# Performance work log

Hardware: AMD Instinct MI355X
Metric: run time of the kernel (lower is better)

## Reference

```python
import jax, jax.numpy as jnp
import numpy as np

C = 64

def setup_inputs() -> dict:
    key = jax.random.key(0)
    ks = jax.random.split(key, 4)
    B, H, W = 16, 256, 256
    feature = jax.random.normal(ks[0], (B, C, H, W), dtype=jnp.float32)
    confidence = jax.random.uniform(ks[1], (B, 1, H, W), dtype=jnp.float32)
    # input_proj: Conv1d(C, C, k=1) -> weight squeezed to [C, C]; state_proj likewise
    Wi = jax.random.normal(ks[2], (C, C), dtype=jnp.float32) * 0.05
    bi = jnp.zeros((C,), dtype=jnp.float32)
    Ws = jax.random.normal(ks[3], (C, C), dtype=jnp.float32) * 0.05
    bs = jnp.zeros((C,), dtype=jnp.float32)
    bias = jnp.zeros((C,), dtype=jnp.float32)
    return {"feature": feature, "confidence": confidence, "Wi": Wi, "bi": bi,
            "Ws": Ws, "bs": bs, "bias": bias}


def reference(feature, confidence, Wi, bi, Ws, bs, bias):
    # direction = 'lr' (propagate left-to-right along width)
    B, Cc, H, W = feature.shape
    # [B,C,H,W] -> [B*H, C, W]  (independent rows)
    seq = feature.transpose(0, 2, 1, 3).reshape(B * H, Cc, W)
    gate = confidence.transpose(0, 2, 1, 3).reshape(B * H, 1, W)
    # pointwise input projection (Conv1d k=1)
    proj = jnp.einsum('oc,ncw->now', Wi, seq) + bi[None, :, None]
    xs = (jnp.moveaxis(proj, -1, 0), jnp.moveaxis(gate, -1, 0))  # [W,N,C], [W,N,1]

    def step(prev, x):
        p_t, g_t = x                      # [N,C], [N,1]
        rec = (prev * g_t) @ Ws.T + bs    # state_proj on gated previous state
        cur = jax.nn.relu(p_t + rec + bias)
        return cur, cur

    init = jnp.zeros((B * H, Cc), dtype=feature.dtype)
    _, ys = jax.lax.scan(step, init, xs)  # [W, N, C]
    out = jnp.moveaxis(ys, 0, -1).reshape(B, H, Cc, W).transpose(0, 2, 1, 3)
    return out
```

## Files before the change

### kernel.cpp

```cpp
#include <hip/hip_runtime.h>
#include <hip/hip_bf16.h>


typedef __attribute__((ext_vector_type(8))) short short8;
typedef __attribute__((ext_vector_type(4))) short short4v;
typedef __attribute__((ext_vector_type(2))) short short2v;
typedef __attribute__((ext_vector_type(4))) float f32x4;

union FragU { unsigned int u[4]; short8 v; };
union PkU { unsigned int u; short2v s2; };

__device__ __forceinline__ unsigned int pk2(float a, float b) {
    unsigned short lo = __bfloat16_as_ushort(__float2bfloat16(a));
    unsigned short hi = __bfloat16_as_ushort(__float2bfloat16(b));
    return (unsigned int)lo | ((unsigned int)hi << 16);
}
__device__ __forceinline__ float b2f(short x) {
    return __uint_as_float(((unsigned int)(unsigned short)x) << 16);
}

__device__ __forceinline__ int fsi(int w, int n, int c) {
    return (w * 1024 + n * 64 + c) ^ ((n & 7) << 3);
}
__device__ __forceinline__ int ogi(int o, int n, int w) {
    return (o * 256 + n * 16 + w) ^ ((((o >> 2) ^ (n >> 2)) & 3) << 2);
}

#define BAR() asm volatile("s_waitcnt lgkmcnt(0)\n\ts_barrier" ::: "memory")

template<int V> struct Ic { static constexpr int value = V; };

__global__ __launch_bounds__(256, 1) void dp_v5_kernel(
    const float* __restrict__ feat, const float* __restrict__ conf,
    const float* __restrict__ Wi, const float* __restrict__ bi,
    const float* __restrict__ Ws, const float* __restrict__ bs,
    const float* __restrict__ bias, float* __restrict__ outp)
{
    __shared__ unsigned short fs[2][16384];
    __shared__ unsigned short og[2][16384];

    const int tid = threadIdx.x;
    const int lane = tid & 63;
    const int wid = tid >> 6;
    const int l15 = lane & 15, g4 = lane >> 4;
    const int nb = blockIdx.x;
    const int b = nb >> 4, h0 = (nb & 15) * 16;

    const float* fb = feat + (size_t)b * 64 * 65536 + (size_t)h0 * 256;

    if (wid == 0) {
        const float* gb = conf + ((size_t)(b * 256) + h0 + l15) * 256;

        FragU Ai[4][2], As[4][2];
        #pragma unroll
        for (int t = 0; t < 4; ++t)
            #pragma unroll
            for (int h = 0; h < 2; ++h) {
                const float* si = Wi + (16 * t + l15) * 64 + 32 * h + g4 * 8;
                const float* ss = Ws + (16 * t + l15) * 64;
                #pragma unroll
                for (int d = 0; d < 4; ++d) {
                    Ai[t][h].u[d] = pk2(si[2 * d], si[2 * d + 1]);
                    const int c0 = 16 * (2 * h + (d >> 1)) + 4 * g4 + 2 * (d & 1);
                    As[t][h].u[d] = pk2(ss[c0], ss[c0 + 1]);
                }
            }
        f32x4 binit[4];
        #pragma unroll
        for (int t = 0; t < 4; ++t)
            #pragma unroll
            for (int r = 0; r < 4; ++r) {
                int o = 16 * t + 4 * g4 + r;
                binit[t][r] = bi[o] + bs[o] + bias[o];
            }

        f32x4 gqA[4], gqB[4];
        #pragma unroll
        for (int q = 0; q < 4; ++q) gqA[q] = *(const f32x4*)(gb + 4 * q);

        FragU S0, S1;
        #pragma unroll
        for (int d = 0; d < 4; ++d) { S0.u[d] = 0u; S1.u[d] = 0u; }

        float curE[4][4];

        BAR();

        auto run_chunk = [&](auto pc, int cc) {
            constexpr int P = decltype(pc)::value;
            f32x4 (&gqc)[4] = P ? gqB : gqA;
            f32x4 (&gqn)[4] = P ? gqA : gqB;
            const int w0 = cc * 16;
            #pragma unroll
            for (int u = 0; u < 16; ++u) {
                short8 F0 = *(const short8*)&fs[P][fsi(u, l15, 8 * g4)];
                short8 F1 = *(const short8*)&fs[P][fsi(u, l15, 32 + 8 * g4)];

                if (u == 2 && cc < 15) {
                    #pragma unroll
                    for (int q = 0; q < 4; ++q)
                        gqn[q] = *(const f32x4*)(gb + w0 + 16 + 4 * q);
                }

                f32x4 a0 = binit[0], a1 = binit[1], a2 = binit[2], a3 = binit[3];
                a0 = __builtin_amdgcn_mfma_f32_16x16x32_bf16(Ai[0][0].v, F0, a0, 0, 0, 0);
                a1 = __builtin_amdgcn_mfma_f32_16x16x32_bf16(Ai[1][0].v, F0, a1, 0, 0, 0);
                a2 = __builtin_amdgcn_mfma_f32_16x16x32_bf16(Ai[2][0].v, F0, a2, 0, 0, 0);
                a3 = __builtin_amdgcn_mfma_f32_16x16x32_bf16(Ai[3][0].v, F0, a3, 0, 0, 0);
                a0 = __builtin_amdgcn_mfma_f32_16x16x32_bf16(Ai[0][1].v, F1, a0, 0, 0, 0);
                a1 = __builtin_amdgcn_mfma_f32_16x16x32_bf16(Ai[1][1].v, F1, a1, 0, 0, 0);
                a2 = __builtin_amdgcn_mfma_f32_16x16x32_bf16(Ai[2][1].v, F1, a2, 0, 0, 0);
                a3 = __builtin_amdgcn_mfma_f32_16x16x32_bf16(Ai[3][1].v, F1, a3, 0, 0, 0);
                a0 = __builtin_amdgcn_mfma_f32_16x16x32_bf16(As[0][0].v, S0.v, a0, 0, 0, 0);
                a1 = __builtin_amdgcn_mfma_f32_16x16x32_bf16(As[1][0].v, S0.v, a1, 0, 0, 0);
                a2 = __builtin_amdgcn_mfma_f32_16x16x32_bf16(As[2][0].v, S0.v, a2, 0, 0, 0);
                a3 = __builtin_amdgcn_mfma_f32_16x16x32_bf16(As[3][0].v, S0.v, a3, 0, 0, 0);
                a0 = __builtin_amdgcn_mfma_f32_16x16x32_bf16(As[0][1].v, S1.v, a0, 0, 0, 0);
                a1 = __builtin_amdgcn_mfma_f32_16x16x32_bf16(As[1][1].v, S1.v, a1, 0, 0, 0);
                a2 = __builtin_amdgcn_mfma_f32_16x16x32_bf16(As[2][1].v, S1.v, a2, 0, 0, 0);
                a3 = __builtin_amdgcn_mfma_f32_16x16x32_bf16(As[3][1].v, S1.v, a3, 0, 0, 0);

                float cur[4][4];
                #pragma unroll
                for (int r = 0; r < 4; ++r) {
                    cur[0][r] = fmaxf(a0[r], 0.f);
                    cur[1][r] = fmaxf(a1[r], 0.f);
                    cur[2][r] = fmaxf(a2[r], 0.f);
                    cur[3][r] = fmaxf(a3[r], 0.f);
                }

                if ((u & 1) == 0) {
                    #pragma unroll
                    for (int t = 0; t < 4; ++t)
                        #pragma unroll
                        for (int r = 0; r < 4; ++r) curE[t][r] = cur[t][r];
                } else {
                    #pragma unroll
                    for (int t = 0; t < 4; ++t)
                        #pragma unroll
                        for (int r = 0; r < 4; ++r) {
                            PkU pk; pk.u = pk2(curE[t][r], cur[t][r]);
                            *(short2v*)&og[P][ogi(16 * t + 4 * g4 + r, l15, u - 1)] = pk.s2;
                        }
                }

                if (!(cc == 15 && u == 15)) {
                    float gv = (u < 15) ? gqc[(u + 1) >> 2][(u + 1) & 3] : gqn[0][0];
                    float g0[4], g1[4], g2[4], g3[4];
                    #pragma unroll
                    for (int r = 0; r < 4; ++r) {
                        g0[r] = cur[0][r] * gv; g1[r] = cur[1][r] * gv;
                        g2[r] = cur[2][r] * gv; g3[r] = cur[3][r] * gv;
                    }
                    S0.u[0] = pk2(g0[0], g0[1]); S0.u[1] = pk2(g0[2], g0[3]);
                    S0.u[2] = pk2(g1[0], g1[1]); S0.u[3] = pk2(g1[2], g1[3]);
                    S1.u[0] = pk2(g2[0], g2[1]); S1.u[1] = pk2(g2[2], g2[3]);
                    S1.u[2] = pk2(g3[0], g3[1]); S1.u[3] = pk2(g3[2], g3[3]);
                }
            }
            BAR();
        };

        #pragma unroll 1
        for (int c2 = 0; c2 < 8; ++c2) {
            run_chunk(Ic<0>{}, 2 * c2);
            run_chunk(Ic<1>{}, 2 * c2 + 1);
        }
    } else if (wid <= 2) {
        const int cb2 = (wid - 1) * 16;
        const int n = lane & 15;

        auto stage = [&](int buf, int w0) {
            f32x4 ra[4][2][4];
            #pragma unroll
            for (int pi = 0; pi < 4; ++pi) {
                const int cp = cb2 + 4 * pi + g4;
                const float* p0 = fb + (size_t)(2 * cp) * 65536 + n * 256 + w0;
                #pragma unroll
                for (int row = 0; row < 2; ++row)
                    #pragma unroll
                    for (int q = 0; q < 4; ++q)
                        ra[pi][row][q] = *(const f32x4*)(p0 + row * 65536 + 4 * q);
            }
            #pragma unroll
            for (int pi = 0; pi < 4; ++pi) {
                const int cp = cb2 + 4 * pi + g4;
                #pragma unroll
                for (int q = 0; q < 4; ++q)
                    #pragma unroll
                    for (int e = 0; e < 4; ++e) {
                        PkU pk; pk.u = pk2(ra[pi][0][q][e], ra[pi][1][q][e]);
                        *(short2v*)&fs[buf][fsi(4 * q + e, n, 2 * cp)] = pk.s2;
                    }
            }
        };

        stage(0, 0);
        BAR();
        #pragma unroll 1
        for (int cc = 0; cc < 16; ++cc) {
            if (cc < 15) stage((cc + 1) & 1, (cc + 1) * 16);
            BAR();
        }
    } else {
        const int n = (lane >> 2) & 15, wq = lane & 3;
        float* const ob = outp + ((size_t)(b * 64) * 256 + h0 + n) * 256 + 4 * wq;

        auto drain = [&](int buf, int wpr) {
            #pragma unroll 8
            for (int o = 0; o < 64; ++o) {
                short4v d = *(const short4v*)&og[buf][ogi(o, n, 4 * wq)];
                f32x4 o4 = { b2f(d.x), b2f(d.y), b2f(d.z), b2f(d.w) };
                *(f32x4*)(ob + (size_t)o * 65536 + wpr) = o4;
            }
        };

        BAR();
        #pragma unroll 1
        for (int cc = 0; cc < 16; ++cc) {
            if (cc > 0) drain((cc - 1) & 1, (cc - 1) * 16);
            BAR();
        }
        drain(1, 240);
    }
}

extern "C" void kernel_launch(void* const* d_in, const int* in_sizes, int n_in,
                              void* d_out, int out_size, void* d_ws, size_t ws_size,
                              hipStream_t stream) {
    const float* feat = (const float*)d_in[0];
    const float* conf = (const float*)d_in[1];
    const float* Wi   = (const float*)d_in[2];
    const float* bi   = (const float*)d_in[3];
    const float* Ws   = (const float*)d_in[4];
    const float* bs   = (const float*)d_in[5];
    const float* bias = (const float*)d_in[6];
    float* out = (float*)d_out;
    (void)d_ws; (void)ws_size; (void)in_sizes; (void)n_in; (void)out_size;

    dp_v5_kernel<<<256, 256, 0, stream>>>(feat, conf, Wi, bi, Ws, bs, bias, out);
}
```

Measured before the change: 184.3 us.

## Move input projection GEMM to producer waves, feed fp32 projections via LDS

The input projection (Wi·x + biases) leaves the serial recurrence wave and moves to the two loader waves. They compute it with MFMA per half-chunk of 8 columns and store fp32 results in a swizzled LDS buffer. The recurrence wave then only runs the Ws MFMAs per step, shortening the critical dependent chain. In exchange the loaders issue scalar strided global loads, and barriers now occur every half-chunk, so the drain wave splits its work across four barriers per chunk pair.

After: 204.6 us. 11.0% more time.

```diff
diff --git a/kernel.cpp b/kernel.cpp
--- a/kernel.cpp
+++ b/kernel.cpp
@@ -19,8 +19,8 @@
     return __uint_as_float(((unsigned int)(unsigned short)x) << 16);
 }
 
-__device__ __forceinline__ int fsi(int w, int n, int c) {
-    return (w * 1024 + n * 64 + c) ^ ((n & 7) << 3);
+__device__ __forceinline__ int psi(int w, int n, int o) {
+    return (w * 1024 + n * 64 + o) ^ ((n & 7) << 2) ^ ((w & 7) << 2);
 }
 __device__ __forceinline__ int ogi(int o, int n, int w) {
     return (o * 256 + n * 16 + w) ^ ((((o >> 2) ^ (n >> 2)) & 3) << 2);
@@ -30,13 +30,13 @@
 
 template<int V> struct Ic { static constexpr int value = V; };
 
-__global__ __launch_bounds__(256, 1) void dp_v5_kernel(
+__global__ __launch_bounds__(256, 1) void dp_v8_kernel(
     const float* __restrict__ feat, const float* __restrict__ conf,
     const float* __restrict__ Wi, const float* __restrict__ bi,
     const float* __restrict__ Ws, const float* __restrict__ bs,
     const float* __restrict__ bias, float* __restrict__ outp)
 {
-    __shared__ unsigned short fs[2][16384];
+    __shared__ float ps[2][8192];
     __shared__ unsigned short og[2][16384];
 
     const int tid = threadIdx.x;
@@ -51,28 +51,18 @@
     if (wid == 0) {
         const float* gb = conf + ((size_t)(b * 256) + h0 + l15) * 256;
 
-        FragU Ai[4][2], As[4][2];
+        FragU As[4][2];
         #pragma unroll
         for (int t = 0; t < 4; ++t)
             #pragma unroll
             for (int h = 0; h < 2; ++h) {
-                const float* si = Wi + (16 * t + l15) * 64 + 32 * h + g4 * 8;
                 const float* ss = Ws + (16 * t + l15) * 64;
                 #pragma unroll
                 for (int d = 0; d < 4; ++d) {
-                    Ai[t][h].u[d] = pk2(si[2 * d], si[2 * d + 1]);
                     const int c0 = 16 * (2 * h + (d >> 1)) + 4 * g4 + 2 * (d & 1);
                     As[t][h].u[d] = pk2(ss[c0], ss[c0 + 1]);
                 }
             }
-        f32x4 binit[4];
-        #pragma unroll
-        for (int t = 0; t < 4; ++t)
-            #pragma unroll
-            for (int r = 0; r < 4; ++r) {
-                int o = 16 * t + 4 * g4 + r;
-                binit[t][r] = bi[o] + bs[o] + bias[o];
-            }
 
         f32x4 gqA[4], gqB[4];
         #pragma unroll
@@ -86,31 +76,32 @@
 
         BAR();
 
-        auto run_chunk = [&](auto pc, int cc) {
-            constexpr int P = decltype(pc)::value;
-            f32x4 (&gqc)[4] = P ? gqB : gqA;
-            f32x4 (&gqn)[4] = P ? gqA : gqB;
-            const int w0 = cc * 16;
-            #pragma unroll
-            for (int u = 0; u < 16; ++u) {
-                short8 F0 = *(const short8*)&fs[P][fsi(u, l15, 8 * g4)];
-                short8 F1 = *(const short8*)&fs[P][fsi(u, l15, 32 + 8 * g4)];
-
-                if (u == 2 && cc < 15) {
+        auto run_half = [&](auto Hc, auto Qc, int C) {
+            constexpr int H = decltype(Hc)::value;
+            constexpr int Q = decltype(Qc)::value;
+            f32x4 (&gqc)[4] = Q ? gqB : gqA;
+            f32x4 (&gqn)[4] = Q ? gqA : gqB;
+            f32x4 accP[2][4];
+            #pragma unroll
+            for (int t = 0; t < 4; ++t)
+                accP[0][t] = *(const f32x4*)&ps[H][psi(0, l15, 16 * t + 4 * g4)];
+            #pragma unroll
+            for (int u = 0; u < 8; ++u) {
+                const int wl = H * 8 + u;
+                if (u < 7) {
+                    #pragma unroll
+                    for (int t = 0; t < 4; ++t)
+                        accP[(u + 1) & 1][t] =
+                            *(const f32x4*)&ps[H][psi(u + 1, l15, 16 * t + 4 * g4)];
+                }
+                if (H == 0 && u == 4 && C < 15) {
                     #pragma unroll
                     for (int q = 0; q < 4; ++q)
-                        gqn[q] = *(const f32x4*)(gb + w0 + 16 + 4 * q);
-                }
-
-                f32x4 a0 = binit[0], a1 = binit[1], a2 = binit[2], a3 = binit[3];
-                a0 = __builtin_amdgcn_mfma_f32_16x16x32_bf16(Ai[0][0].v, F0, a0, 0, 0, 0);
-                a1 = __builtin_amdgcn_mfma_f32_16x16x32_bf16(Ai[1][0].v, F0, a1, 0, 0, 0);
-                a2 = __builtin_amdgcn_mfma_f32_16x16x32_bf16(Ai[2][0].v, F0, a2, 0, 0, 0);
-                a3 = __builtin_amdgcn_mfma_f32_16x16x32_bf16(Ai[3][0].v, F0, a3, 0, 0, 0);
-                a0 = __builtin_amdgcn_mfma_f32_16x16x32_bf16(Ai[0][1].v, F1, a0, 0, 0, 0);
-                a1 = __builtin_amdgcn_mfma_f32_16x16x32_bf16(Ai[1][1].v, F1, a1, 0, 0, 0);
-                a2 = __builtin_amdgcn_mfma_f32_16x16x32_bf16(Ai[2][1].v, F1, a2, 0, 0, 0);
-                a3 = __builtin_amdgcn_mfma_f32_16x16x32_bf16(Ai[3][1].v, F1, a3, 0, 0, 0);
+                        gqn[q] = *(const f32x4*)(gb + (C + 1) * 16 + 4 * q);
+                }
+
+                f32x4 a0 = accP[u & 1][0], a1 = accP[u & 1][1];
+                f32x4 a2 = accP[u & 1][2], a3 = accP[u & 1][3];
                 a0 = __builtin_amdgcn_mfma_f32_16x16x32_bf16(As[0][0].v, S0.v, a0, 0, 0, 0);
                 a1 = __builtin_amdgcn_mfma_f32_16x16x32_bf16(As[1][0].v, S0.v, a1, 0, 0, 0);
                 a2 = __builtin_amdgcn_mfma_f32_16x16x32_bf16(As[2][0].v, S0.v, a2, 0, 0, 0);
@@ -129,7 +120,7 @@
                     cur[3][r] = fmaxf(a3[r], 0.f);
                 }
 
-                if ((u & 1) == 0) {
+                if ((wl & 1) == 0) {
                     #pragma unroll
                     for (int t = 0; t < 4; ++t)
                         #pragma unroll
@@ -140,12 +131,12 @@
                         #pragma unroll
                         for (int r = 0; r < 4; ++r) {
                             PkU pk; pk.u = pk2(curE[t][r], cur[t][r]);
-                            *(short2v*)&og[P][ogi(16 * t + 4 * g4 + r, l15, u - 1)] = pk.s2;
+                            *(short2v*)&og[Q][ogi(16 * t + 4 * g4 + r, l15, wl - 1)] = pk.s2;
                         }
                 }
 
-                if (!(cc == 15 && u == 15)) {
-                    float gv = (u < 15) ? gqc[(u + 1) >> 2][(u + 1) & 3] : gqn[0][0];
+                if (!(C == 15 && wl == 15)) {
+                    float gv = (wl < 15) ? gqc[(wl + 1) >> 2][(wl + 1) & 3] : gqn[0][0];
                     float g0[4], g1[4], g2[4], g3[4];
                     #pragma unroll
                     for (int r = 0; r < 4; ++r) {
@@ -163,52 +154,88 @@
 
         #pragma unroll 1
         for (int c2 = 0; c2 < 8; ++c2) {
-            run_chunk(Ic<0>{}, 2 * c2);
-            run_chunk(Ic<1>{}, 2 * c2 + 1);
+            const int C0 = 2 * c2, C1 = 2 * c2 + 1;
+            run_half(Ic<0>{}, Ic<0>{}, C0);
+            run_half(Ic<1>{}, Ic<0>{}, C0);
+            run_half(Ic<0>{}, Ic<1>{}, C1);
+            run_half(Ic<1>{}, Ic<1>{}, C1);
         }
     } else if (wid <= 2) {
-        const int cb2 = (wid - 1) * 16;
-        const int n = lane & 15;
-
-        auto stage = [&](int buf, int w0) {
-            f32x4 ra[4][2][4];
-            #pragma unroll
-            for (int pi = 0; pi < 4; ++pi) {
-                const int cp = cb2 + 4 * pi + g4;
-                const float* p0 = fb + (size_t)(2 * cp) * 65536 + n * 256 + w0;
-                #pragma unroll
-                for (int row = 0; row < 2; ++row)
-                    #pragma unroll
-                    for (int q = 0; q < 4; ++q)
-                        ra[pi][row][q] = *(const f32x4*)(p0 + row * 65536 + 4 * q);
-            }
-            #pragma unroll
-            for (int pi = 0; pi < 4; ++pi) {
-                const int cp = cb2 + 4 * pi + g4;
-                #pragma unroll
-                for (int q = 0; q < 4; ++q)
-                    #pragma unroll
-                    for (int e = 0; e < 4; ++e) {
-                        PkU pk; pk.u = pk2(ra[pi][0][q][e], ra[pi][1][q][e]);
-                        *(short2v*)&fs[buf][fsi(4 * q + e, n, 2 * cp)] = pk.s2;
+        const int nb8 = (wid - 1) * 8;
+        const int n2 = l15 >> 3, wq8 = l15 & 7;
+
+        FragU Ai[4][2];
+        #pragma unroll
+        for (int t = 0; t < 4; ++t)
+            #pragma unroll
+            for (int h = 0; h < 2; ++h) {
+                const float* si = Wi + (16 * t + l15) * 64 + 32 * h + g4 * 8;
+                #pragma unroll
+                for (int d = 0; d < 4; ++d)
+                    Ai[t][h].u[d] = pk2(si[2 * d], si[2 * d + 1]);
+            }
+        f32x4 binit[4];
+        #pragma unroll
+        for (int t = 0; t < 4; ++t)
+            #pragma unroll
+            for (int r = 0; r < 4; ++r) {
+                int o = 16 * t + 4 * g4 + r;
+                binit[t][r] = bi[o] + bs[o] + bias[o];
+            }
+
+        float fr[4][16];
+        auto issue_loads = [&](int w0) {
+            #pragma unroll
+            for (int ng = 0; ng < 4; ++ng) {
+                const int nL = nb8 + 2 * ng + n2;
+                const float* base = fb + (size_t)nL * 256 + w0 + wq8;
+                #pragma unroll
+                for (int hh = 0; hh < 2; ++hh)
+                    #pragma unroll
+                    for (int d = 0; d < 4; ++d) {
+                        const int c0 = 32 * hh + 8 * g4 + 2 * d;
+                        fr[ng][hh * 8 + 2 * d]     = base[(size_t)c0 * 65536];
+                        fr[ng][hh * 8 + 2 * d + 1] = base[(size_t)(c0 + 1) * 65536];
                     }
             }
         };
-
-        stage(0, 0);
+        auto compute_ps = [&](int buf) {
+            #pragma unroll
+            for (int ng = 0; ng < 4; ++ng) {
+                const int nL = nb8 + 2 * ng + n2;
+                FragU B0, B1;
+                #pragma unroll
+                for (int d = 0; d < 4; ++d) {
+                    B0.u[d] = pk2(fr[ng][2 * d],     fr[ng][2 * d + 1]);
+                    B1.u[d] = pk2(fr[ng][8 + 2 * d], fr[ng][8 + 2 * d + 1]);
+                }
+                #pragma unroll
+                for (int t = 0; t < 4; ++t) {
+                    f32x4 acc = binit[t];
+                    acc = __builtin_amdgcn_mfma_f32_16x16x32_bf16(Ai[t][0].v, B0.v, acc, 0, 0, 0);
+                    acc = __builtin_amdgcn_mfma_f32_16x16x32_bf16(Ai[t][1].v, B1.v, acc, 0, 0, 0);
+                    *(f32x4*)&ps[buf][psi(wq8, nL, 16 * t + 4 * g4)] = acc;
+                }
+            }
+        };
+
+        issue_loads(0);
+        compute_ps(0);
+        issue_loads(8);
         BAR();
         #pragma unroll 1
-        for (int cc = 0; cc < 16; ++cc) {
-            if (cc < 15) stage((cc + 1) & 1, (cc + 1) * 16);
+        for (int hc = 0; hc < 32; ++hc) {
+            if (hc < 31) compute_ps((hc + 1) & 1);
+            if (hc < 30) issue_loads((hc + 2) * 8);
             BAR();
         }
     } else {
         const int n = (lane >> 2) & 15, wq = lane & 3;
         float* const ob = outp + ((size_t)(b * 64) * 256 + h0 + n) * 256 + 4 * wq;
 
-        auto drain = [&](int buf, int wpr) {
+        auto drain_half = [&](int buf, int wpr, int o0) {
             #pragma unroll 8
-            for (int o = 0; o < 64; ++o) {
+            for (int o = o0; o < o0 + 32; ++o) {
                 short4v d = *(const short4v*)&og[buf][ogi(o, n, 4 * wq)];
                 f32x4 o4 = { b2f(d.x), b2f(d.y), b2f(d.z), b2f(d.w) };
                 *(f32x4*)(ob + (size_t)o * 65536 + wpr) = o4;
@@ -217,11 +244,19 @@
 
         BAR();
         #pragma unroll 1
-        for (int cc = 0; cc < 16; ++cc) {
-            if (cc > 0) drain((cc - 1) & 1, (cc - 1) * 16);
+        for (int c2 = 0; c2 < 8; ++c2) {
+            const int C0 = 2 * c2;
+            if (c2 > 0) drain_half(1, (C0 - 1) * 16, 0);
+            BAR();
+            if (c2 > 0) drain_half(1, (C0 - 1) * 16, 32);
+            BAR();
+            drain_half(0, C0 * 16, 0);
+            BAR();
+            drain_half(0, C0 * 16, 32);
             BAR();
         }
-        drain(1, 240);
+        drain_half(1, 240, 0);
+        drain_half(1, 240, 32);
     }
 }
 
@@ -238,5 +273,5 @@
     float* out = (float*)d_out;
     (void)d_ws; (void)ws_size; (void)in_sizes; (void)n_in; (void)out_size;
 
-    dp_v5_kernel<<<256, 256, 0, stream>>>(feat, conf, Wi, bi, Ws, bs, bias, out);
-}
+    dp_v8_kernel<<<256, 256, 0, stream>>>(feat, conf, Wi, bi, Ws, bs, bias, out);
+}
```

## Offload gate loads to drain warp via LDS and software-pipeline fragment reads

Applied to the files above, without the earlier changes.

Confidence gate values are now loaded by the output-drain warp and written into a four-slot LDS ring, so the serial recurrence warp no longer issues global loads. The compute loop becomes a rolled pair-step loop that prefetches the next timestep's feature fragments and gate value one step ahead, using precomputed swizzled offsets. This takes global latency off the critical recurrence path and shrinks the instruction footprint. The cost is extra LDS traffic, and the rolled loop may add loop overhead or schedule worse than full unrolling.

New measurement: 187.6 us. No clear change (+1.8%).

```diff
diff --git a/kernel.cpp b/kernel.cpp
--- a/kernel.cpp
+++ b/kernel.cpp
@@ -28,9 +28,7 @@
 
 #define BAR() asm volatile("s_waitcnt lgkmcnt(0)\n\ts_barrier" ::: "memory")
 
-template<int V> struct Ic { static constexpr int value = V; };
-
-__global__ __launch_bounds__(256, 1) void dp_v5_kernel(
+__global__ __launch_bounds__(256, 1) void dp_v9_kernel(
     const float* __restrict__ feat, const float* __restrict__ conf,
     const float* __restrict__ Wi, const float* __restrict__ bi,
     const float* __restrict__ Ws, const float* __restrict__ bs,
@@ -38,6 +36,7 @@
 {
     __shared__ unsigned short fs[2][16384];
     __shared__ unsigned short og[2][16384];
+    __shared__ float gs[4][256];
 
     const int tid = threadIdx.x;
     const int lane = tid & 63;
@@ -49,8 +48,6 @@
     const float* fb = feat + (size_t)b * 64 * 65536 + (size_t)h0 * 256;
 
     if (wid == 0) {
-        const float* gb = conf + ((size_t)(b * 256) + h0 + l15) * 256;
-
         FragU Ai[4][2], As[4][2];
         #pragma unroll
         for (int t = 0; t < 4; ++t)
@@ -74,97 +71,106 @@
                 binit[t][r] = bi[o] + bs[o] + bias[o];
             }
 
-        f32x4 gqA[4], gqB[4];
-        #pragma unroll
-        for (int q = 0; q < 4; ++q) gqA[q] = *(const f32x4*)(gb + 4 * q);
-
         FragU S0, S1;
         #pragma unroll
         for (int d = 0; d < 4; ++d) { S0.u[d] = 0u; S1.u[d] = 0u; }
 
+        const int fo0 = (l15 * 64 + 8 * g4) ^ ((l15 & 7) << 3);
+        const int fo1 = (l15 * 64 + 32 + 8 * g4) ^ ((l15 & 7) << 3);
+        const int swz = ((g4 ^ (l15 >> 2)) & 3) << 2;
+        const int ogl = g4 * 1024 + l15 * 16;
+
         float curE[4][4];
 
+        auto mstep = [&](const short8& F0, const short8& F1, float (&cur)[4][4]) {
+            f32x4 a0 = binit[0], a1 = binit[1], a2 = binit[2], a3 = binit[3];
+            a0 = __builtin_amdgcn_mfma_f32_16x16x32_bf16(Ai[0][0].v, F0, a0, 0, 0, 0);
+            a1 = __builtin_amdgcn_mfma_f32_16x16x32_bf16(Ai[1][0].v, F0, a1, 0, 0, 0);
+            a2 = __builtin_amdgcn_mfma_f32_16x16x32_bf16(Ai[2][0].v, F0, a2, 0, 0, 0);
+            a3 = __builtin_amdgcn_mfma_f32_16x16x32_bf16(Ai[3][0].v, F0, a3, 0, 0, 0);
+            a0 = __builtin_amdgcn_mfma_f32_16x16x32_bf16(Ai[0][1].v, F1, a0, 0, 0, 0);
+            a1 = __builtin_amdgcn_mfma_f32_16x16x32_bf16(Ai[1][1].v, F1, a1, 0, 0, 0);
+            a2 = __builtin_amdgcn_mfma_f32_16x16x32_bf16(Ai[2][1].v, F1, a2, 0, 0, 0);
+            a3 = __builtin_amdgcn_mfma_f32_16x16x32_bf16(Ai[3][1].v, F1, a3, 0, 0, 0);
+            a0 = __builtin_amdgcn_mfma_f32_16x16x32_bf16(As[0][0].v, S0.v, a0, 0, 0, 0);
+            a1 = __builtin_amdgcn_mfma_f32_16x16x32_bf16(As[1][0].v, S0.v, a1, 0, 0, 0);
+            a2 = __builtin_amdgcn_mfma_f32_16x16x32_bf16(As[2][0].v, S0.v, a2, 0, 0, 0);
+            a3 = __builtin_amdgcn_mfma_f32_16x16x32_bf16(As[3][0].v, S0.v, a3, 0, 0, 0);
+            a0 = __builtin_amdgcn_mfma_f32_16x16x32_bf16(As[0][1].v, S1.v, a0, 0, 0, 0);
+            a1 = __builtin_amdgcn_mfma_f32_16x16x32_bf16(As[1][1].v, S1.v, a1, 0, 0, 0);
+            a2 = __builtin_amdgcn_mfma_f32_16x16x32_bf16(As[2][1].v, S1.v, a2, 0, 0, 0);
+            a3 = __builtin_amdgcn_mfma_f32_16x16x32_bf16(As[3][1].v, S1.v, a3, 0, 0, 0);
+            #pragma unroll
+            for (int r = 0; r < 4; ++r) {
+                cur[0][r] = fmaxf(a0[r], 0.f);
+                cur[1][r] = fmaxf(a1[r], 0.f);
+                cur[2][r] = fmaxf(a2[r], 0.f);
+                cur[3][r] = fmaxf(a3[r], 0.f);
+            }
+        };
+        auto rebuild = [&](const float (&cur)[4][4], float gv) {
+            float g0[4], g1[4], g2[4], g3[4];
+            #pragma unroll
+            for (int r = 0; r < 4; ++r) {
+                g0[r] = cur[0][r] * gv; g1[r] = cur[1][r] * gv;
+                g2[r] = cur[2][r] * gv; g3[r] = cur[3][r] * gv;
+            }
+            S0.u[0] = pk2(g0[0], g0[1]); S0.u[1] = pk2(g0[2], g0[3]);
+            S0.u[2] = pk2(g1[0], g1[1]); S0.u[3] = pk2(g1[2], g1[3]);
+            S1.u[0] = pk2(g2[0], g2[1]); S1.u[1] = pk2(g2[2], g2[3]);
+            S1.u[2] = pk2(g3[0], g3[1]); S1.u[3] = pk2(g3[2], g3[3]);
+        };
+
         BAR();
 
-        auto run_chunk = [&](auto pc, int cc) {
-            constexpr int P = decltype(pc)::value;
-            f32x4 (&gqc)[4] = P ? gqB : gqA;
-            f32x4 (&gqn)[4] = P ? gqA : gqB;
-            const int w0 = cc * 16;
-            #pragma unroll
-            for (int u = 0; u < 16; ++u) {
-                short8 F0 = *(const short8*)&fs[P][fsi(u, l15, 8 * g4)];
-                short8 F1 = *(const short8*)&fs[P][fsi(u, l15, 32 + 8 * g4)];
-
-                if (u == 2 && cc < 15) {
-                    #pragma unroll
-                    for (int q = 0; q < 4; ++q)
-                        gqn[q] = *(const f32x4*)(gb + w0 + 16 + 4 * q);
-                }
-
-                f32x4 a0 = binit[0], a1 = binit[1], a2 = binit[2], a3 = binit[3];
-                a0 = __builtin_amdgcn_mfma_f32_16x16x32_bf16(Ai[0][0].v, F0, a0, 0, 0, 0);
-                a1 = __builtin_amdgcn_mfma_f32_16x16x32_bf16(Ai[1][0].v, F0, a1, 0, 0, 0);
-                a2 = __builtin_amdgcn_mfma_f32_16x16x32_bf16(Ai[2][0].v, F0, a2, 0, 0, 0);
-                a3 = __builtin_amdgcn_mfma_f32_16x16x32_bf16(Ai[3][0].v, F0, a3, 0, 0, 0);
-                a0 = __builtin_amdgcn_mfma_f32_16x16x32_bf16(Ai[0][1].v, F1, a0, 0, 0, 0);
-                a1 = __builtin_amdgcn_mfma_f32_16x16x32_bf16(Ai[1][1].v, F1, a1, 0, 0, 0);
-                a2 = __builtin_amdgcn_mfma_f32_16x16x32_bf16(Ai[2][1].v, F1, a2, 0, 0, 0);
-                a3 = __builtin_amdgcn_mfma_f32_16x16x32_bf16(Ai[3][1].v, F1, a3, 0, 0, 0);
-                a0 = __builtin_amdgcn_mfma_f32_16x16x32_bf16(As[0][0].v, S0.v, a0, 0, 0, 0);
-                a1 = __builtin_amdgcn_mfma_f32_16x16x32_bf16(As[1][0].v, S0.v, a1, 0, 0, 0);
-                a2 = __builtin_amdgcn_mfma_f32_16x16x32_bf16(As[2][0].v, S0.v, a2, 0, 0, 0);
-                a3 = __builtin_amdgcn_mfma_f32_16x16x32_bf16(As[3][0].v, S0.v, a3, 0, 0, 0);
-                a0 = __builtin_amdgcn_mfma_f32_16x16x32_bf16(As[0][1].v, S1.v, a0, 0, 0, 0);
-                a1 = __builtin_amdgcn_mfma_f32_16x16x32_bf16(As[1][1].v, S1.v, a1, 0, 0, 0);
-                a2 = __builtin_amdgcn_mfma_f32_16x16x32_bf16(As[2][1].v, S1.v, a2, 0, 0, 0);
-                a3 = __builtin_amdgcn_mfma_f32_16x16x32_bf16(As[3][1].v, S1.v, a3, 0, 0, 0);
-
-                float cur[4][4];
-                #pragma unroll
-                for (int r = 0; r < 4; ++r) {
-                    cur[0][r] = fmaxf(a0[r], 0.f);
-                    cur[1][r] = fmaxf(a1[r], 0.f);
-                    cur[2][r] = fmaxf(a2[r], 0.f);
-                    cur[3][r] = fmaxf(a3[r], 0.f);
-                }
-
-                if ((u & 1) == 0) {
+        #pragma unroll 1
+        for (int cc = 0; cc < 16; ++cc) {
+            const unsigned short* fsb = fs[cc & 1];
+            unsigned short* ogb = og[cc & 1];
+            const float* gsc = gs[cc & 3];
+            const float* gsn = gs[(cc + 1) & 3];
+
+            short8 Fn0 = *(const short8*)&fsb[fo0];
+            short8 Fn1 = *(const short8*)&fsb[fo1];
+
+            #pragma unroll 1
+            for (int up = 0; up < 8; ++up) {
+                {
+                    const int u = 2 * up;
+                    short8 F0 = Fn0, F1 = Fn1;
+                    Fn0 = *(const short8*)&fsb[(u + 1) * 1024 + fo0];
+                    Fn1 = *(const short8*)&fsb[(u + 1) * 1024 + fo1];
+                    float gvn = gsc[(u + 1) * 16 + l15];
+                    float cur[4][4];
+                    mstep(F0, F1, cur);
                     #pragma unroll
                     for (int t = 0; t < 4; ++t)
                         #pragma unroll
                         for (int r = 0; r < 4; ++r) curE[t][r] = cur[t][r];
-                } else {
+                    rebuild(cur, gvn);
+                }
+                {
+                    const int u = 2 * up + 1;
+                    short8 F0 = Fn0, F1 = Fn1;
+                    if (up < 7) {
+                        Fn0 = *(const short8*)&fsb[(u + 1) * 1024 + fo0];
+                        Fn1 = *(const short8*)&fsb[(u + 1) * 1024 + fo1];
+                    }
+                    float gvn = (up < 7) ? gsc[(u + 1) * 16 + l15] : gsn[l15];
+                    float cur[4][4];
+                    mstep(F0, F1, cur);
+                    unsigned short* opb = ogb + ogl + ((u - 1) ^ swz);
                     #pragma unroll
                     for (int t = 0; t < 4; ++t)
                         #pragma unroll
                         for (int r = 0; r < 4; ++r) {
                             PkU pk; pk.u = pk2(curE[t][r], cur[t][r]);
-                            *(short2v*)&og[P][ogi(16 * t + 4 * g4 + r, l15, u - 1)] = pk.s2;
+                            *(short2v*)&opb[t * 4096 + r * 256] = pk.s2;
                         }
+                    if (!(cc == 15 && up == 7)) rebuild(cur, gvn);
                 }
-
-                if (!(cc == 15 && u == 15)) {
-                    float gv = (u < 15) ? gqc[(u + 1) >> 2][(u + 1) & 3] : gqn[0][0];
-                    float g0[4], g1[4], g2[4], g3[4];
-                    #pragma unroll
-                    for (int r = 0; r < 4; ++r) {
-                        g0[r] = cur[0][r] * gv; g1[r] = cur[1][r] * gv;
-                        g2[r] = cur[2][r] * gv; g3[r] = cur[3][r] * gv;
-                    }
-                    S0.u[0] = pk2(g0[0], g0[1]); S0.u[1] = pk2(g0[2], g0[3]);
-                    S0.u[2] = pk2(g1[0], g1[1]); S0.u[3] = pk2(g1[2], g1[3]);
-                    S1.u[0] = pk2(g2[0], g2[1]); S1.u[1] = pk2(g2[2], g2[3]);
-                    S1.u[2] = pk2(g3[0], g3[1]); S1.u[3] = pk2(g3[2], g3[3]);
-                }
             }
             BAR();
-        };
-
-        #pragma unroll 1
-        for (int c2 = 0; c2 < 8; ++c2) {
-            run_chunk(Ic<0>{}, 2 * c2);
-            run_chunk(Ic<1>{}, 2 * c2 + 1);
         }
     } else if (wid <= 2) {
         const int cb2 = (wid - 1) * 16;
@@ -205,6 +211,7 @@
     } else {
         const int n = (lane >> 2) & 15, wq = lane & 3;
         float* const ob = outp + ((size_t)(b * 64) * 256 + h0 + n) * 256 + 4 * wq;
+        const float* const gbd = conf + ((size_t)(b * 256) + h0 + n) * 256;
 
         auto drain = [&](int buf, int wpr) {
             #pragma unroll 8
@@ -214,11 +221,20 @@
                 *(f32x4*)(ob + (size_t)o * 65536 + wpr) = o4;
             }
         };
-
+        auto stage_gs = [&](int k) {
+            f32x4 v = *(const f32x4*)(gbd + 16 * k + 4 * wq);
+            float* gd = gs[k & 3];
+            #pragma unroll
+            for (int e = 0; e < 4; ++e) gd[(4 * wq + e) * 16 + n] = v[e];
+        };
+
+        stage_gs(0);
+        stage_gs(1);
         BAR();
         #pragma unroll 1
         for (int cc = 0; cc < 16; ++cc) {
             if (cc > 0) drain((cc - 1) & 1, (cc - 1) * 16);
+            if (cc < 14) stage_gs(cc + 2);
             BAR();
         }
         drain(1, 240);
@@ -238,5 +254,5 @@
     float* out = (float*)d_out;
     (void)d_ws; (void)ws_size; (void)in_sizes; (void)n_in; (void)out_size;
 
-    dp_v5_kernel<<<256, 256, 0, stream>>>(feat, conf, Wi, bi, Ws, bs, bias, out);
-}
+    dp_v9_kernel<<<256, 256, 0, stream>>>(feat, conf, Wi, bi, Ws, bs, bias, out);
+}
```

## Write outputs from compute wave, stage gates in LDS, double chunk width

Applied to the files above, without the earlier changes.

The compute wave now writes fp32 outputs straight to global memory in groups of four timesteps, and the LDS output buffer and drain wave are removed. The freed wave stages confidence gates into LDS. Chunks grow from 16 to 32 timesteps, which halves the number of barriers. The compute wave also prefetches the next timestep's feature fragment from LDS. The intent is to cut barrier count, keep outputs in fp32 rather than rounding them to bf16 and back, and move global gate loads off the serial recurrence path. The cost is that the latency-critical wave now issues global stores itself, and the loader waves write LDS with scalar 16-bit stores.

Result: slower. 325.4 us (+76.5%).

```diff
diff --git a/kernel.cpp b/kernel.cpp
--- a/kernel.cpp
+++ b/kernel.cpp
@@ -3,41 +3,26 @@
 
 
 typedef __attribute__((ext_vector_type(8))) short short8;
-typedef __attribute__((ext_vector_type(4))) short short4v;
-typedef __attribute__((ext_vector_type(2))) short short2v;
 typedef __attribute__((ext_vector_type(4))) float f32x4;
 
 union FragU { unsigned int u[4]; short8 v; };
-union PkU { unsigned int u; short2v s2; };
 
 __device__ __forceinline__ unsigned int pk2(float a, float b) {
     unsigned short lo = __bfloat16_as_ushort(__float2bfloat16(a));
     unsigned short hi = __bfloat16_as_ushort(__float2bfloat16(b));
     return (unsigned int)lo | ((unsigned int)hi << 16);
 }
-__device__ __forceinline__ float b2f(short x) {
-    return __uint_as_float(((unsigned int)(unsigned short)x) << 16);
-}
-
-__device__ __forceinline__ int fsi(int w, int n, int c) {
-    return (w * 1024 + n * 64 + c) ^ ((n & 7) << 3);
-}
-__device__ __forceinline__ int ogi(int o, int n, int w) {
-    return (o * 256 + n * 16 + w) ^ ((((o >> 2) ^ (n >> 2)) & 3) << 2);
-}
 
 #define BAR() asm volatile("s_waitcnt lgkmcnt(0)\n\ts_barrier" ::: "memory")
 
-template<int V> struct Ic { static constexpr int value = V; };
-
-__global__ __launch_bounds__(256, 1) void dp_v5_kernel(
+__global__ __launch_bounds__(256, 1) void dp_v10_kernel(
     const float* __restrict__ feat, const float* __restrict__ conf,
     const float* __restrict__ Wi, const float* __restrict__ bi,
     const float* __restrict__ Ws, const float* __restrict__ bs,
     const float* __restrict__ bias, float* __restrict__ outp)
 {
-    __shared__ unsigned short fs[2][16384];
-    __shared__ unsigned short og[2][16384];
+    __shared__ unsigned short fs[2][32768];
+    __shared__ float gs[2][512];
 
     const int tid = threadIdx.x;
     const int lane = tid & 63;
@@ -49,8 +34,6 @@
     const float* fb = feat + (size_t)b * 64 * 65536 + (size_t)h0 * 256;
 
     if (wid == 0) {
-        const float* gb = conf + ((size_t)(b * 256) + h0 + l15) * 256;
-
         FragU Ai[4][2], As[4][2];
         #pragma unroll
         for (int t = 0; t < 4; ++t)
@@ -74,154 +57,179 @@
                 binit[t][r] = bi[o] + bs[o] + bias[o];
             }
 
-        f32x4 gqA[4], gqB[4];
-        #pragma unroll
-        for (int q = 0; q < 4; ++q) gqA[q] = *(const f32x4*)(gb + 4 * q);
-
         FragU S0, S1;
         #pragma unroll
         for (int d = 0; d < 4; ++d) { S0.u[d] = 0u; S1.u[d] = 0u; }
 
-        float curE[4][4];
+        const int fo0 = (l15 * 64 + 8 * g4) ^ ((l15 & 7) << 3);
+        const int fo1 = (l15 * 64 + 32 + 8 * g4) ^ ((l15 & 7) << 3);
+        float* const obase = outp + (size_t)(b * 64 + 4 * g4) * 65536
+                                  + (size_t)(h0 + l15) * 256;
+
+        auto mstep = [&](const short8& F0, const short8& F1, float (&cur)[4][4]) {
+            f32x4 a0 = binit[0], a1 = binit[1], a2 = binit[2], a3 = binit[3];
+            a0 = __builtin_amdgcn_mfma_f32_16x16x32_bf16(Ai[0][0].v, F0, a0, 0, 0, 0);
+            a1 = __builtin_amdgcn_mfma_f32_16x16x32_bf16(Ai[1][0].v, F0, a1, 0, 0, 0);
+            a2 = __builtin_amdgcn_mfma_f32_16x16x32_bf16(Ai[2][0].v, F0, a2, 0, 0, 0);
+            a3 = __builtin_amdgcn_mfma_f32_16x16x32_bf16(Ai[3][0].v, F0, a3, 0, 0, 0);
+            a0 = __builtin_amdgcn_mfma_f32_16x16x32_bf16(Ai[0][1].v, F1, a0, 0, 0, 0);
+            a1 = __builtin_amdgcn_mfma_f32_16x16x32_bf16(Ai[1][1].v, F1, a1, 0, 0, 0);
+            a2 = __builtin_amdgcn_mfma_f32_16x16x32_bf16(Ai[2][1].v, F1, a2, 0, 0, 0);
+            a3 = __builtin_amdgcn_mfma_f32_16x16x32_bf16(Ai[3][1].v, F1, a3, 0, 0, 0);
+            a0 = __builtin_amdgcn_mfma_f32_16x16x32_bf16(As[0][0].v, S0.v, a0, 0, 0, 0);
+            a1 = __builtin_amdgcn_mfma_f32_16x16x32_bf16(As[1][0].v, S0.v, a1, 0, 0, 0);
+            a2 = __builtin_amdgcn_mfma_f32_16x16x32_bf16(As[2][0].v, S0.v, a2, 0, 0, 0);
+            a3 = __builtin_amdgcn_mfma_f32_16x16x32_bf16(As[3][0].v, S0.v, a3, 0, 0, 0);
+            a0 = __builtin_amdgcn_mfma_f32_16x16x32_bf16(As[0][1].v, S1.v, a0, 0, 0, 0);
+            a1 = __builtin_amdgcn_mfma_f32_16x16x32_bf16(As[1][1].v, S1.v, a1, 0, 0, 0);
+            a2 = __builtin_amdgcn_mfma_f32_16x16x32_bf16(As[2][1].v, S1.v, a2, 0, 0, 0);
+            a3 = __builtin_amdgcn_mfma_f32_16x16x32_bf16(As[3][1].v, S1.v, a3, 0, 0, 0);
+            #pragma unroll
+            for (int r = 0; r < 4; ++r) {
+                cur[0][r] = fmaxf(a0[r], 0.f);
+                cur[1][r] = fmaxf(a1[r], 0.f);
+                cur[2][r] = fmaxf(a2[r], 0.f);
+                cur[3][r] = fmaxf(a3[r], 0.f);
+            }
+        };
+        auto rebuild = [&](const float (&cur)[4][4], float gv) {
+            float g0[4], g1[4], g2[4], g3[4];
+            #pragma unroll
+            for (int r = 0; r < 4; ++r) {
+                g0[r] = cur[0][r] * gv; g1[r] = cur[1][r] * gv;
+                g2[r] = cur[2][r] * gv; g3[r] = cur[3][r] * gv;
+            }
+            S0.u[0] = pk2(g0[0], g0[1]); S0.u[1] = pk2(g0[2], g0[3]);
+            S0.u[2] = pk2(g1[0], g1[1]); S0.u[3] = pk2(g1[2], g1[3]);
+            S1.u[0] = pk2(g2[0], g2[1]); S1.u[1] = pk2(g2[2], g2[3]);
+            S1.u[2] = pk2(g3[0], g3[1]); S1.u[3] = pk2(g3[2], g3[3]);
+        };
+
+        float curQ[4][4][4];
+        float pend[4][4];
 
         BAR();
 
-        auto run_chunk = [&](auto pc, int cc) {
-            constexpr int P = decltype(pc)::value;
-            f32x4 (&gqc)[4] = P ? gqB : gqA;
-            f32x4 (&gqn)[4] = P ? gqA : gqB;
-            const int w0 = cc * 16;
-            #pragma unroll
-            for (int u = 0; u < 16; ++u) {
-                short8 F0 = *(const short8*)&fs[P][fsi(u, l15, 8 * g4)];
-                short8 F1 = *(const short8*)&fs[P][fsi(u, l15, 32 + 8 * g4)];
-
-                if (u == 2 && cc < 15) {
-                    #pragma unroll
-                    for (int q = 0; q < 4; ++q)
-                        gqn[q] = *(const f32x4*)(gb + w0 + 16 + 4 * q);
-                }
-
-                f32x4 a0 = binit[0], a1 = binit[1], a2 = binit[2], a3 = binit[3];
-                a0 = __builtin_amdgcn_mfma_f32_16x16x32_bf16(Ai[0][0].v, F0, a0, 0, 0, 0);
-                a1 = __builtin_amdgcn_mfma_f32_16x16x32_bf16(Ai[1][0].v, F0, a1, 0, 0, 0);
-                a2 = __builtin_amdgcn_mfma_f32_16x16x32_bf16(Ai[2][0].v, F0, a2, 0, 0, 0);
-                a3 = __builtin_amdgcn_mfma_f32_16x16x32_bf16(Ai[3][0].v, F0, a3, 0, 0, 0);
-                a0 = __builtin_amdgcn_mfma_f32_16x16x32_bf16(Ai[0][1].v, F1, a0, 0, 0, 0);
-                a1 = __builtin_amdgcn_mfma_f32_16x16x32_bf16(Ai[1][1].v, F1, a1, 0, 0, 0);
-                a2 = __builtin_amdgcn_mfma_f32_16x16x32_bf16(Ai[2][1].v, F1, a2, 0, 0, 0);
-                a3 = __builtin_amdgcn_mfma_f32_16x16x32_bf16(Ai[3][1].v, F1, a3, 0, 0, 0);
-                a0 = __builtin_amdgcn_mfma_f32_16x16x32_bf16(As[0][0].v, S0.v, a0, 0, 0, 0);
-                a1 = __builtin_amdgcn_mfma_f32_16x16x32_bf16(As[1][0].v, S0.v, a1, 0, 0, 0);
-                a2 = __builtin_amdgcn_mfma_f32_16x16x32_bf16(As[2][0].v, S0.v, a2, 0, 0, 0);
-                a3 = __builtin_amdgcn_mfma_f32_16x16x32_bf16(As[3][0].v, S0.v, a3, 0, 0, 0);
-                a0 = __builtin_amdgcn_mfma_f32_16x16x32_bf16(As[0][1].v, S1.v, a0, 0, 0, 0);
-                a1 = __builtin_amdgcn_mfma_f32_16x16x32_bf16(As[1][1].v, S1.v, a1, 0, 0, 0);
-                a2 = __builtin_amdgcn_mfma_f32_16x16x32_bf16(As[2][1].v, S1.v, a2, 0, 0, 0);
-                a3 = __builtin_amdgcn_mfma_f32_16x16x32_bf16(As[3][1].v, S1.v, a3, 0, 0, 0);
-
-                float cur[4][4];
-                #pragma unroll
-                for (int r = 0; r < 4; ++r) {
-                    cur[0][r] = fmaxf(a0[r], 0.f);
-                    cur[1][r] = fmaxf(a1[r], 0.f);
-                    cur[2][r] = fmaxf(a2[r], 0.f);
-                    cur[3][r] = fmaxf(a3[r], 0.f);
-                }
-
-                if ((u & 1) == 0) {
+        #pragma unroll 1
+        for (int sc = 0; sc < 8; ++sc) {
+            const unsigned short* fsb = fs[sc & 1];
+            const float* gsb = gs[sc & 1];
+            if (sc > 0) rebuild(pend, gsb[l15]);
+            short8 Fn0 = *(const short8*)&fsb[fo0];
+            short8 Fn1 = *(const short8*)&fsb[fo1];
+
+            #pragma unroll 1
+            for (int up = 0; up < 8; ++up) {
+                #pragma unroll
+                for (int q = 0; q < 4; ++q) {
+                    const int u = 4 * up + q;
+                    short8 F0 = Fn0, F1 = Fn1;
+                    if (u < 31) {
+                        const int w1 = u + 1;
+                        const int sw = (w1 & 7) << 3;
+                        Fn0 = *(const short8*)&fsb[w1 * 1024 + (fo0 ^ sw)];
+                        Fn1 = *(const short8*)&fsb[w1 * 1024 + (fo1 ^ sw)];
+                    }
+                    float cur[4][4];
+                    mstep(F0, F1, cur);
                     #pragma unroll
                     for (int t = 0; t < 4; ++t)
                         #pragma unroll
-                        for (int r = 0; r < 4; ++r) curE[t][r] = cur[t][r];
-                } else {
-                    #pragma unroll
-                    for (int t = 0; t < 4; ++t)
+                        for (int r = 0; r < 4; ++r) curQ[t][r][q] = cur[t][r];
+                    if (u < 31) {
+                        rebuild(cur, gsb[(u + 1) * 16 + l15]);
+                    } else {
                         #pragma unroll
-                        for (int r = 0; r < 4; ++r) {
-                            PkU pk; pk.u = pk2(curE[t][r], cur[t][r]);
-                            *(short2v*)&og[P][ogi(16 * t + 4 * g4 + r, l15, u - 1)] = pk.s2;
-                        }
+                        for (int t = 0; t < 4; ++t)
+                            #pragma unroll
+                            for (int r = 0; r < 4; ++r) pend[t][r] = cur[t][r];
+                    }
                 }
-
-                if (!(cc == 15 && u == 15)) {
-                    float gv = (u < 15) ? gqc[(u + 1) >> 2][(u + 1) & 3] : gqn[0][0];
-                    float g0[4], g1[4], g2[4], g3[4];
+                const int w0g = sc * 32 + 4 * up;
+                #pragma unroll
+                for (int t = 0; t < 4; ++t)
                     #pragma unroll
                     for (int r = 0; r < 4; ++r) {
-                        g0[r] = cur[0][r] * gv; g1[r] = cur[1][r] * gv;
-                        g2[r] = cur[2][r] * gv; g3[r] = cur[3][r] * gv;
-                    }
-                    S0.u[0] = pk2(g0[0], g0[1]); S0.u[1] = pk2(g0[2], g0[3]);
-                    S0.u[2] = pk2(g1[0], g1[1]); S0.u[3] = pk2(g1[2], g1[3]);
-                    S1.u[0] = pk2(g2[0], g2[1]); S1.u[1] = pk2(g2[2], g2[3]);
-                    S1.u[2] = pk2(g3[0], g3[1]); S1.u[3] = pk2(g3[2], g3[3]);
-                }
+                        f32x4 v = { curQ[t][r][0], curQ[t][r][1],
+                                    curQ[t][r][2], curQ[t][r][3] };
+                        *(f32x4*)(obase + (size_t)(16 * t + r) * 65536 + w0g) = v;
+                    }
             }
             BAR();
-        };
-
-        #pragma unroll 1
-        for (int c2 = 0; c2 < 8; ++c2) {
-            run_chunk(Ic<0>{}, 2 * c2);
-            run_chunk(Ic<1>{}, 2 * c2 + 1);
         }
     } else if (wid <= 2) {
-        const int cb2 = (wid - 1) * 16;
-        const int n = lane & 15;
-
-        auto stage = [&](int buf, int w0) {
-            f32x4 ra[4][2][4];
-            #pragma unroll
-            for (int pi = 0; pi < 4; ++pi) {
-                const int cp = cb2 + 4 * pi + g4;
-                const float* p0 = fb + (size_t)(2 * cp) * 65536 + n * 256 + w0;
-                #pragma unroll
-                for (int row = 0; row < 2; ++row)
-                    #pragma unroll
-                    for (int q = 0; q < 4; ++q)
-                        ra[pi][row][q] = *(const f32x4*)(p0 + row * 65536 + 4 * q);
-            }
-            #pragma unroll
-            for (int pi = 0; pi < 4; ++pi) {
-                const int cp = cb2 + 4 * pi + g4;
-                #pragma unroll
-                for (int q = 0; q < 4; ++q)
+        const int cb = (wid - 1) * 32;
+        const int rr = lane >> 3, ll = lane & 7;
+
+        auto ldg = [&](f32x4 (&ra)[2][4], int g, int w0) {
+            #pragma unroll
+            for (int nn = 0; nn < 2; ++nn)
+                #pragma unroll
+                for (int ci = 0; ci < 4; ++ci)
+                    ra[nn][ci] = *(const f32x4*)(fb
+                        + (size_t)(cb + 8 * ci + rr) * 65536
+                        + (2 * g + nn) * 256 + w0 + 4 * ll);
+        };
+        auto wrg = [&](const f32x4 (&ra)[2][4], int g, unsigned short* half) {
+            #pragma unroll
+            for (int nn = 0; nn < 2; ++nn) {
+                const int n = 2 * g + nn;
+                #pragma unroll
+                for (int ci = 0; ci < 4; ++ci) {
+                    const int c = cb + 8 * ci + rr;
+                    const int base = (n * 64 + c) ^ ((n & 7) << 3);
                     #pragma unroll
                     for (int e = 0; e < 4; ++e) {
-                        PkU pk; pk.u = pk2(ra[pi][0][q][e], ra[pi][1][q][e]);
-                        *(short2v*)&fs[buf][fsi(4 * q + e, n, 2 * cp)] = pk.s2;
-                    }
+                        const int w = 4 * ll + e;
+                        half[w * 1024 + (base ^ ((w & 7) << 3))] =
+                            __bfloat16_as_ushort(__float2bfloat16(ra[nn][ci][e]));
+                    }
+                }
+            }
+        };
+        auto stage = [&](int hb, int w0) {
+            unsigned short* half = fs[hb];
+            f32x4 ra0[2][4], ra1[2][4];
+            ldg(ra0, 0, w0);
+            ldg(ra1, 1, w0);
+            #pragma unroll 1
+            for (int g2 = 0; g2 < 4; ++g2) {
+                wrg(ra0, 2 * g2, half);
+                if (g2 < 3) ldg(ra0, 2 * g2 + 2, w0);
+                wrg(ra1, 2 * g2 + 1, half);
+                if (g2 < 3) ldg(ra1, 2 * g2 + 3, w0);
             }
         };
 
         stage(0, 0);
         BAR();
         #pragma unroll 1
-        for (int cc = 0; cc < 16; ++cc) {
-            if (cc < 15) stage((cc + 1) & 1, (cc + 1) * 16);
+        for (int k = 0; k < 8; ++k) {
+            if (k < 7) stage((k + 1) & 1, (k + 1) * 32);
             BAR();
         }
     } else {
-        const int n = (lane >> 2) & 15, wq = lane & 3;
-        float* const ob = outp + ((size_t)(b * 64) * 256 + h0 + n) * 256 + 4 * wq;
-
-        auto drain = [&](int buf, int wpr) {
-            #pragma unroll 8
-            for (int o = 0; o < 64; ++o) {
-                short4v d = *(const short4v*)&og[buf][ogi(o, n, 4 * wq)];
-                f32x4 o4 = { b2f(d.x), b2f(d.y), b2f(d.z), b2f(d.w) };
-                *(f32x4*)(ob + (size_t)o * 65536 + wpr) = o4;
-            }
-        };
-
+        const int n = lane >> 2, qq = lane & 3;
+        const float* const gbd = conf + ((size_t)(b * 256) + h0 + n) * 256;
+
+        auto stage_g = [&](int hb, int w0) {
+            f32x4 v0 = *(const f32x4*)(gbd + w0 + 4 * qq);
+            f32x4 v1 = *(const f32x4*)(gbd + w0 + 16 + 4 * qq);
+            float* gd = gs[hb];
+            #pragma unroll
+            for (int e = 0; e < 4; ++e) {
+                gd[(4 * qq + e) * 16 + n] = v0[e];
+                gd[(16 + 4 * qq + e) * 16 + n] = v1[e];
+            }
+        };
+
+        stage_g(0, 0);
         BAR();
         #pragma unroll 1
-        for (int cc = 0; cc < 16; ++cc) {
-            if (cc > 0) drain((cc - 1) & 1, (cc - 1) * 16);
+        for (int k = 0; k < 8; ++k) {
+            if (k < 7) stage_g((k + 1) & 1, (k + 1) * 32);
             BAR();
         }
-        drain(1, 240);
     }
 }
 
@@ -238,5 +246,5 @@
     float* out = (float*)d_out;
     (void)d_ws; (void)ws_size; (void)in_sizes; (void)n_in; (void)out_size;
 
-    dp_v5_kernel<<<256, 256, 0, stream>>>(feat, conf, Wi, bi, Ws, bs, bias, out);
+    dp_v10_kernel<<<256, 256, 0, stream>>>(feat, conf, Wi, bi, Ws, bs, bias, out);
 }
```
